# Kernel optimization log

Measured on AMD Instinct MI355X. Metric: run time of the kernel, lower is better.

Reference implementation:

```python
import jax, jax.numpy as jnp
import numpy as np


def setup_inputs() -> dict:
    key = jax.random.key(0)
    ks = jax.random.split(key, 6)
    B, C1, C2, C, H, W = 16, 512, 320, 256, 64, 64
    x1 = jax.random.normal(ks[0], (B, C1, H, W), dtype=jnp.float32)
    x2 = jax.random.normal(ks[1], (B, C2, H, W), dtype=jnp.float32)
    # 1x1 conv weights, bias=False -> plain channel matmuls
    w_img = jax.random.normal(ks[2], (C, C1), dtype=jnp.float32) * (1.0 / np.sqrt(C1))
    w_txt = jax.random.normal(ks[3], (C, C2), dtype=jnp.float32) * (1.0 / np.sqrt(C2))
    w_out = jax.random.normal(ks[4], (C1, C), dtype=jnp.float32) * (1.0 / np.sqrt(C))
    gamma = jax.random.normal(ks[5], (1,), dtype=jnp.float32)
    return {"x1": x1, "x2": x2, "w_img": w_img, "w_txt": w_txt,
            "w_out": w_out, "gamma": gamma}


def reference(x1, x2, w_img, w_txt, w_out, gamma):
    B, _, H, W = x1.shape
    # 1x1 conv projections (bias-free) == channel matmuls
    img = jnp.einsum('oc,bchw->bohw', w_img, x1)   # [B,C,H,W]
    txt = jnp.einsum('oc,bchw->bohw', w_txt, x2)   # [B,C,H,W]
    C = img.shape[1]
    q = img.reshape(B, C, H * W)                    # [B,C,N]
    kv = txt.reshape(B, C, H * W)                   # [B,C,N]
    attn = jnp.einsum('bcn,bdn->bcd', q, kv)        # QK^T over spatial dim
    attn = jax.nn.softmax(attn, axis=-1)            # [B,C,C]
    attn_info = jnp.einsum('bcd,bdn->bcn', attn, kv).reshape(B, C, H, W)
    out = gamma[0] * attn_info + img                # scale-residual
    out = jnp.einsum('oc,bchw->bohw', w_out, out)   # output 1x1 conv
    return out
```

## Files before the change

kernel.cpp:

```cpp
#include <hip/hip_runtime.h>
#include <stdint.h>

typedef _Float16 f16_t;
typedef _Float16 f16x4 __attribute__((ext_vector_type(4)));
typedef _Float16 f16x8 __attribute__((ext_vector_type(8)));
typedef float f32x4 __attribute__((ext_vector_type(4)));

__device__ __forceinline__ void async16(const void* g, void* lds) {
    typedef __attribute__((address_space(3))) void lds_void;
    typedef __attribute__((address_space(1))) void glb_void;
    lds_void* l = (lds_void*)(unsigned int)(unsigned long long)lds;
    glb_void* gp = (glb_void*)(unsigned long long)g;
    __builtin_amdgcn_global_load_lds(gp, l, 16, 0, 0);
}

__global__ void cvt3(const float* __restrict__ a, f16_t* __restrict__ oa, int na,
                     const float* __restrict__ b, f16_t* __restrict__ ob, int nb,
                     const float* __restrict__ c, f16_t* __restrict__ oc, int nc) {
    int i = blockIdx.x * 256 + threadIdx.x;
    if (i < na) oa[i] = (f16_t)a[i];
    if (i < nb) ob[i] = (f16_t)b[i];
    if (i < nc) oc[i] = (f16_t)c[i];
}

template <int BM, int BN, int TM, int TN, int WM, int WN, int MODE, int KSPLIT, int FUSET>
__global__ __launch_bounds__(256, 2)
void gemm_bt(const f16_t* __restrict__ A, const f16_t* __restrict__ B16,
             const float* __restrict__ Bf32,
             void* __restrict__ C, const f16_t* __restrict__ resid,
             const float* __restrict__ gamma, f16_t* __restrict__ Ct,
             int M, int N, int K,
             long long strideA, long long strideB, long long strideC,
             long long strideCt) {
    constexpr int BK = 32;
    static_assert(FUSET == 0 || (BN == 128), "fused path assumes BN=128");
    constexpr int ASZ = BM * BK;
    constexpr int BSZ = BN * BK;
    constexpr int STG = 2 * ASZ + 2 * BSZ;
    constexpr int LT = (MODE == 3) ? BN * (BM + 8) : 0;
    constexpr int POOL = (STG > LT) ? STG : LT;
    __shared__ __align__(16) f16_t pool[POOL];

    const int tid = threadIdx.x;
    const int wave = tid >> 6;
    const int lane = tid & 63;
    const int wm = wave / WN;
    const int wn = wave % WN;
    const int l16 = lane & 15;
    const int l4 = lane >> 4;

    const long long zb = (KSPLIT == 1) ? blockIdx.z : (blockIdx.z / KSPLIT);
    const int ks = (KSPLIT == 1) ? 0 : (blockIdx.z % KSPLIT);
    const int Ksl = K / KSPLIT;
    const f16_t* Ab = A + zb * strideA + (long long)blockIdx.y * BM * K;
    const f16_t* Bb = (FUSET == 0) ? (B16 + zb * strideB + (long long)blockIdx.x * BN * K) : nullptr;
    const float* BfB = FUSET ? (Bf32 + zb * strideB + blockIdx.x * BN) : nullptr;

    f32x4 zero = {0.f, 0.f, 0.f, 0.f};
    f32x4 acc[TM][TN];
#pragma unroll
    for (int i = 0; i < TM; ++i)
#pragma unroll
        for (int j = 0; j < TN; ++j) acc[i][j] = zero;

    auto stageA = [&](int b, int k0) {
        f16_t* As = pool + b * ASZ;
#pragma unroll
        for (int r = 0; r < (BM * 4) / 256; ++r) {
            int seg = r * 256 + tid;
            const f16_t* g = Ab + (long long)(seg >> 2) * K + k0 + (seg & 3) * 8;
            async16(g, &As[(r * 256 + wave * 64) * 8]);
        }
    };
    auto stageB16 = [&](int b, int k0) {
#pragma unroll
        for (int r = 0; r < (BN * 4) / 256; ++r) {
            int seg = r * 256 + tid;
            const f16_t* g = Bb + (long long)(seg >> 2) * K + k0 + (seg & 3) * 8;
            async16(g, &pool[2 * ASZ + b * BSZ + (r * 256 + wave * 64) * 8]);
        }
    };
    float4 br[4];
    const int fk = tid >> 3;
    const int fc = (tid & 7) * 4;
    const int fswz = ((fk >> 3) & 3) * 8;
    auto loadB = [&](int k0) {
#pragma unroll
        for (int i = 0; i < 4; ++i)
            br[i] = *(const float4*)(BfB + (long long)(k0 + fk) * N + fc + i * 32);
    };
    auto writeB = [&](int b) {
        f16_t* Bs = pool + 2 * ASZ + b * BSZ;
#pragma unroll
        for (int i = 0; i < 4; ++i) {
            int n4 = fc + i * 32;
            f16x4 h;
            h[0] = (f16_t)br[i].x; h[1] = (f16_t)br[i].y;
            h[2] = (f16_t)br[i].z; h[3] = (f16_t)br[i].w;
            *(f16x4*)&Bs[fk * BN + (n4 ^ fswz)] = h;
        }
    };

    auto compute = [&](int b) {
        const f16_t* As = pool + b * ASZ;
        f16x8 af[TM], bfr[TN];
#pragma unroll
        for (int i = 0; i < TM; ++i)
            af[i] = *(const f16x8*)&As[((wm * TM + i) * 16 + l16) * BK + l4 * 8];
        if (FUSET) {
            const f16_t* Bs = pool + 2 * ASZ + b * BSZ;
#pragma unroll
            for (int j = 0; j < TN; ++j) {
                const int nj = ((wn * TN + j) * 16 + l16) ^ (l4 * 8);
                f16x8 t;
#pragma unroll
                for (int e = 0; e < 8; ++e)
                    t[e] = Bs[(l4 * 8 + e) * BN + nj];
                bfr[j] = t;
            }
        } else {
            const f16_t* Bs = pool + 2 * ASZ + b * BSZ;
#pragma unroll
            for (int j = 0; j < TN; ++j)
                bfr[j] = *(const f16x8*)&Bs[((wn * TN + j) * 16 + l16) * BK + l4 * 8];
        }
#pragma unroll
        for (int i = 0; i < TM; ++i)
#pragma unroll
            for (int j = 0; j < TN; ++j)
                acc[i][j] = __builtin_amdgcn_mfma_f32_16x16x32_f16(af[i], bfr[j], acc[i][j], 0, 0, 0);
    };

    const int kBeg = ks * Ksl;
    const int NT = Ksl / BK;
    int cur = 0;
    if (FUSET) {
        loadB(kBeg);
        stageA(0, kBeg);
        writeB(0);
        __syncthreads();
        for (int t = 1; t < NT; ++t) {
            loadB(kBeg + t * BK);
            stageA(cur ^ 1, kBeg + t * BK);
            compute(cur);
            writeB(cur ^ 1);
            __syncthreads();
            cur ^= 1;
        }
        compute(cur);
    } else {
        stageA(0, kBeg);
        stageB16(0, kBeg);
        __syncthreads();
        for (int t = 1; t < NT; ++t) {
            stageA(cur ^ 1, kBeg + t * BK);
            stageB16(cur ^ 1, kBeg + t * BK);
            compute(cur);
            __syncthreads();
            cur ^= 1;
        }
        compute(cur);
    }

    if (MODE == 3) __syncthreads();

    const int row0 = blockIdx.y * BM + wm * TM * 16;
    const int col0 = blockIdx.x * BN + wn * TN * 16;
    float g = (MODE == 2) ? gamma[0] : 0.f;
#pragma unroll
    for (int i = 0; i < TM; ++i) {
#pragma unroll
        for (int j = 0; j < TN; ++j) {
            f16x4 tq;
#pragma unroll
            for (int r = 0; r < 4; ++r) {
                int row = row0 + i * 16 + l4 * 4 + r;
                int col = col0 + j * 16 + l16;
                float v = acc[i][j][r];
                if (MODE == 4) {
                    long long idx = (long long)blockIdx.z * strideC + (long long)row * N + col;
                    ((float*)C)[idx] = v;
                } else {
                    long long idx = zb * strideC + (long long)row * N + col;
                    if (MODE == 0) {
                        ((f16_t*)C)[idx] = (f16_t)v;
                    } else if (MODE == 1) {
                        ((float*)C)[idx] = v;
                    } else if (MODE == 2) {
                        float im = (float)resid[idx];
                        ((f16_t*)C)[idx] = (f16_t)(g * v + im);
                    } else if (MODE == 3) {
                        ((f16_t*)C)[idx] = (f16_t)v;
                        tq[r] = (f16_t)v;
                    }
                }
            }
            if (MODE == 3) {
                int rl = wm * (TM * 16) + i * 16 + l4 * 4;
                int cl = wn * (TN * 16) + j * 16 + l16;
                *(f16x4*)&pool[cl * (BM + 8) + rl] = tq;
            }
        }
    }

    if (MODE == 3) {
        __syncthreads();
        const int bx0 = blockIdx.x * BN;
        const int by0 = blockIdx.y * BM;
        const long long cb = zb * strideCt;
        constexpr int TPR = BM / 8;
        constexpr int RPI = 256 / TPR;
#pragma unroll
        for (int it = 0; it < BN / RPI; ++it) {
            int nl = it * RPI + (tid / TPR);
            int c8 = (tid % TPR) * 8;
            f16x8 v = *(const f16x8*)&pool[nl * (BM + 8) + c8];
            *(f16x8*)&Ct[cb + (long long)(bx0 + nl) * M + by0 + c8] = v;
        }
    }
}

template <int KS>
__global__ void softmax_red(const float* __restrict__ part, f16_t* __restrict__ out) {
    const int row = blockIdx.x * 4 + (threadIdx.x >> 6);
    const int lane = threadIdx.x & 63;
    const int b = row >> 8, r = row & 255;
    const float* p = part + (long long)(b * KS) * 65536 + r * 256 + lane * 4;
    float4 v = *(const float4*)p;
#pragma unroll
    for (int k = 1; k < KS; ++k) {
        float4 u = *(const float4*)(p + (long long)k * 65536);
        v.x += u.x; v.y += u.y; v.z += u.z; v.w += u.w;
    }
    float m = fmaxf(fmaxf(v.x, v.y), fmaxf(v.z, v.w));
#pragma unroll
    for (int off = 32; off > 0; off >>= 1) m = fmaxf(m, __shfl_xor(m, off, 64));
    float e0 = __expf(v.x - m), e1 = __expf(v.y - m);
    float e2 = __expf(v.z - m), e3 = __expf(v.w - m);
    float s = e0 + e1 + e2 + e3;
#pragma unroll
    for (int off = 32; off > 0; off >>= 1) s += __shfl_xor(s, off, 64);
    const float inv = 1.0f / s;
    f16x4 o;
    o[0] = (f16_t)(e0 * inv);
    o[1] = (f16_t)(e1 * inv);
    o[2] = (f16_t)(e2 * inv);
    o[3] = (f16_t)(e3 * inv);
    *(f16x4*)(out + ((long long)row) * 256 + lane * 4) = o;
}

extern "C" void kernel_launch(void* const* d_in, const int* in_sizes, int n_in,
                              void* d_out, int out_size, void* d_ws, size_t ws_size,
                              hipStream_t stream) {
    (void)in_sizes; (void)n_in; (void)out_size; (void)ws_size;

    const float* x1 = (const float*)d_in[0];
    const float* x2 = (const float*)d_in[1];
    const float* w_img = (const float*)d_in[2];
    const float* w_txt = (const float*)d_in[3];
    const float* w_out = (const float*)d_in[4];
    const float* gamma = (const float*)d_in[5];

    constexpr int B = 16, C1 = 512, C2 = 320, C = 256, N = 4096, OC = 512;
    constexpr int KS = 8;
    constexpr long long NC = (long long)N * C;
    constexpr long long CC = (long long)C * C;

    char* ws = (char*)d_ws;
    f16_t* wib   = (f16_t*)(ws + 0);
    f16_t* wtb   = (f16_t*)(ws + 262144);
    f16_t* wob   = (f16_t*)(ws + 425984);
    f16_t* img   = (f16_t*)(ws + 688128);
    f16_t* imgT  = (f16_t*)(ws + 34242560);
    f16_t* kvT   = (f16_t*)(ws + 67796992);
    f16_t* attns = (f16_t*)(ws + 101351424);
    f16_t* yT    = img;

    char* oc = (char*)d_out;
    f16_t* kv   = (f16_t*)(oc);
    float* part = (float*)(oc + 33554432);

    cvt3<<<512, 256, 0, stream>>>(w_img, wib, C * C1, w_txt, wtb, C * C2, w_out, wob, OC * C);

    gemm_bt<256, 128, 8, 4, 2, 2, 3, 1, 1><<<dim3(N / 128, 1, B), 256, 0, stream>>>(
        wib, nullptr, x1, img, nullptr, nullptr, imgT, C, N, C1,
        0LL, (long long)C1 * N, NC, NC);

    gemm_bt<256, 128, 8, 4, 2, 2, 3, 1, 1><<<dim3(N / 128, 1, B), 256, 0, stream>>>(
        wtb, nullptr, x2, kv, nullptr, nullptr, kvT, C, N, C2,
        0LL, (long long)C2 * N, NC, NC);

    gemm_bt<128, 128, 4, 4, 2, 2, 4, KS, 0><<<dim3(C / 128, C / 128, B * KS), 256, 0, stream>>>(
        img, kv, nullptr, part, nullptr, nullptr, nullptr, C, C, N,
        NC, NC, CC, 0LL);

    softmax_red<KS><<<(B * C) / 4, 256, 0, stream>>>(part, attns);

    gemm_bt<128, 128, 4, 4, 2, 2, 2, 1, 0><<<dim3(C / 128, N / 128, B), 256, 0, stream>>>(
        kvT, attns, nullptr, yT, imgT, gamma, nullptr, N, C, C,
        NC, CC, NC, 0LL);

    gemm_bt<256, 128, 8, 4, 2, 2, 1, 1, 0><<<dim3(N / 128, OC / 256, B), 256, 0, stream>>>(
        wob, yT, nullptr, (float*)d_out, nullptr, nullptr, nullptr, OC, N, C,
        0LL, NC, (long long)OC * N, 0LL);
}
```

Measured before the change: 391.9 us.

## Fuse projection GEMMs, convert weights in-kernel, raise K-split, shrink tiles

Replaces the separate weight-conversion kernel with in-GEMM fp32-to-fp16 loading of the A operand, and merges the image and text projection GEMMs into one launch with 128x128 tiles. The QK^T split-K factor goes from 8 to 16 and the output GEMM uses 128-row tiles. Occupancy hint rises to 3 blocks per CU. The aim is fewer launches and more parallel blocks. The cost is that weights are reconverted per block in registers, the A tile in LDS is written unswizzled, and the split-K partials double the reduction traffic.

```diff
diff --git a/kernel.cpp b/kernel.cpp
--- a/kernel.cpp
+++ b/kernel.cpp
@@ -14,32 +14,21 @@
     __builtin_amdgcn_global_load_lds(gp, l, 16, 0, 0);
 }
 
-__global__ void cvt3(const float* __restrict__ a, f16_t* __restrict__ oa, int na,
-                     const float* __restrict__ b, f16_t* __restrict__ ob, int nb,
-                     const float* __restrict__ c, f16_t* __restrict__ oc, int nc) {
-    int i = blockIdx.x * 256 + threadIdx.x;
-    if (i < na) oa[i] = (f16_t)a[i];
-    if (i < nb) ob[i] = (f16_t)b[i];
-    if (i < nc) oc[i] = (f16_t)c[i];
-}
-
-template <int BM, int BN, int TM, int TN, int WM, int WN, int MODE, int KSPLIT, int FUSET>
-__global__ __launch_bounds__(256, 2)
-void gemm_bt(const f16_t* __restrict__ A, const f16_t* __restrict__ B16,
-             const float* __restrict__ Bf32,
-             void* __restrict__ C, const f16_t* __restrict__ resid,
-             const float* __restrict__ gamma, f16_t* __restrict__ Ct,
-             int M, int N, int K,
-             long long strideA, long long strideB, long long strideC,
-             long long strideCt) {
+template <int BM, int BN, int TM, int TN, int WM, int WN, int MODE, int FA, int FB>
+__device__ __forceinline__ void gemm_core(
+    const void* __restrict__ Aop,
+    const void* __restrict__ Bop,
+    void* __restrict__ C,
+    const f16_t* __restrict__ resid,
+    const float* __restrict__ gamma,
+    f16_t* __restrict__ Ct,
+    int ldC, int ldCt, int ldA, int ldB,
+    int kBeg, int kEnd, int row0b, int col0b,
+    f16_t* __restrict__ pool) {
     constexpr int BK = 32;
-    static_assert(FUSET == 0 || (BN == 128), "fused path assumes BN=128");
     constexpr int ASZ = BM * BK;
     constexpr int BSZ = BN * BK;
-    constexpr int STG = 2 * ASZ + 2 * BSZ;
-    constexpr int LT = (MODE == 3) ? BN * (BM + 8) : 0;
-    constexpr int POOL = (STG > LT) ? STG : LT;
-    __shared__ __align__(16) f16_t pool[POOL];
+    static_assert(FB == 0 || BN == 128, "fused-B path assumes BN=128");
 
     const int tid = threadIdx.x;
     const int wave = tid >> 6;
@@ -49,12 +38,10 @@
     const int l16 = lane & 15;
     const int l4 = lane >> 4;
 
-    const long long zb = (KSPLIT == 1) ? blockIdx.z : (blockIdx.z / KSPLIT);
-    const int ks = (KSPLIT == 1) ? 0 : (blockIdx.z % KSPLIT);
-    const int Ksl = K / KSPLIT;
-    const f16_t* Ab = A + zb * strideA + (long long)blockIdx.y * BM * K;
-    const f16_t* Bb = (FUSET == 0) ? (B16 + zb * strideB + (long long)blockIdx.x * BN * K) : nullptr;
-    const float* BfB = FUSET ? (Bf32 + zb * strideB + blockIdx.x * BN) : nullptr;
+    const f16_t* A16 = (const f16_t*)Aop;
+    const float* A32 = (const float*)Aop;
+    const f16_t* B16 = (const f16_t*)Bop;
+    const float* B32 = (const float*)Bop;
 
     f32x4 zero = {0.f, 0.f, 0.f, 0.f};
     f32x4 acc[TM][TN];
@@ -63,52 +50,79 @@
 #pragma unroll
         for (int j = 0; j < TN; ++j) acc[i][j] = zero;
 
+    float4 ar[FA ? 4 : 1];
+    auto loadA = [&](int k0) {
+        if (FA) {
+#pragma unroll
+            for (int s = 0; s < 4; ++s) {
+                int seg = s * 256 + tid;
+                ar[s] = *(const float4*)(A32 + (long long)(seg >> 3) * ldA + k0 + (seg & 7) * 4);
+            }
+        }
+    };
+    auto writeA = [&](int b) {
+        if (FA) {
+            f16_t* As = pool + b * ASZ;
+#pragma unroll
+            for (int s = 0; s < 4; ++s) {
+                int seg = s * 256 + tid;
+                f16x4 h;
+                h[0] = (f16_t)ar[s].x; h[1] = (f16_t)ar[s].y;
+                h[2] = (f16_t)ar[s].z; h[3] = (f16_t)ar[s].w;
+                *(f16x4*)&As[(seg >> 3) * BK + (seg & 7) * 4] = h;
+            }
+        }
+    };
     auto stageA = [&](int b, int k0) {
         f16_t* As = pool + b * ASZ;
 #pragma unroll
         for (int r = 0; r < (BM * 4) / 256; ++r) {
             int seg = r * 256 + tid;
-            const f16_t* g = Ab + (long long)(seg >> 2) * K + k0 + (seg & 3) * 8;
+            const f16_t* g = A16 + (long long)(seg >> 2) * ldA + k0 + (seg & 3) * 8;
             async16(g, &As[(r * 256 + wave * 64) * 8]);
         }
     };
-    auto stageB16 = [&](int b, int k0) {
-#pragma unroll
-        for (int r = 0; r < (BN * 4) / 256; ++r) {
-            int seg = r * 256 + tid;
-            const f16_t* g = Bb + (long long)(seg >> 2) * K + k0 + (seg & 3) * 8;
-            async16(g, &pool[2 * ASZ + b * BSZ + (r * 256 + wave * 64) * 8]);
-        }
-    };
-    float4 br[4];
+    float4 br[FB ? 4 : 1];
     const int fk = tid >> 3;
     const int fc = (tid & 7) * 4;
     const int fswz = ((fk >> 3) & 3) * 8;
     auto loadB = [&](int k0) {
-#pragma unroll
-        for (int i = 0; i < 4; ++i)
-            br[i] = *(const float4*)(BfB + (long long)(k0 + fk) * N + fc + i * 32);
+        if (FB) {
+#pragma unroll
+            for (int i = 0; i < 4; ++i)
+                br[i] = *(const float4*)(B32 + (long long)(k0 + fk) * ldB + fc + i * 32);
+        }
     };
     auto writeB = [&](int b) {
-        f16_t* Bs = pool + 2 * ASZ + b * BSZ;
-#pragma unroll
-        for (int i = 0; i < 4; ++i) {
-            int n4 = fc + i * 32;
-            f16x4 h;
-            h[0] = (f16_t)br[i].x; h[1] = (f16_t)br[i].y;
-            h[2] = (f16_t)br[i].z; h[3] = (f16_t)br[i].w;
-            *(f16x4*)&Bs[fk * BN + (n4 ^ fswz)] = h;
+        if (FB) {
+            f16_t* Bs = pool + 2 * ASZ + b * BSZ;
+#pragma unroll
+            for (int i = 0; i < 4; ++i) {
+                int n4 = fc + i * 32;
+                f16x4 h;
+                h[0] = (f16_t)br[i].x; h[1] = (f16_t)br[i].y;
+                h[2] = (f16_t)br[i].z; h[3] = (f16_t)br[i].w;
+                *(f16x4*)&Bs[fk * BN + (n4 ^ fswz)] = h;
+            }
+        }
+    };
+    auto stageB = [&](int b, int k0) {
+#pragma unroll
+        for (int r = 0; r < (BN * 4) / 256; ++r) {
+            int seg = r * 256 + tid;
+            const f16_t* g = B16 + (long long)(seg >> 2) * ldB + k0 + (seg & 3) * 8;
+            async16(g, &pool[2 * ASZ + b * BSZ + (r * 256 + wave * 64) * 8]);
         }
     };
 
     auto compute = [&](int b) {
         const f16_t* As = pool + b * ASZ;
+        const f16_t* Bs = pool + 2 * ASZ + b * BSZ;
         f16x8 af[TM], bfr[TN];
 #pragma unroll
         for (int i = 0; i < TM; ++i)
             af[i] = *(const f16x8*)&As[((wm * TM + i) * 16 + l16) * BK + l4 * 8];
-        if (FUSET) {
-            const f16_t* Bs = pool + 2 * ASZ + b * BSZ;
+        if (FB) {
 #pragma unroll
             for (int j = 0; j < TN; ++j) {
                 const int nj = ((wn * TN + j) * 16 + l16) ^ (l4 * 8);
@@ -119,7 +133,6 @@
                 bfr[j] = t;
             }
         } else {
-            const f16_t* Bs = pool + 2 * ASZ + b * BSZ;
 #pragma unroll
             for (int j = 0; j < TN; ++j)
                 bfr[j] = *(const f16x8*)&Bs[((wn * TN + j) * 16 + l16) * BK + l4 * 8];
@@ -131,42 +144,30 @@
                 acc[i][j] = __builtin_amdgcn_mfma_f32_16x16x32_f16(af[i], bfr[j], acc[i][j], 0, 0, 0);
     };
 
-    const int kBeg = ks * Ksl;
-    const int NT = Ksl / BK;
+    const int NT = (kEnd - kBeg) / BK;
     int cur = 0;
-    if (FUSET) {
-        loadB(kBeg);
-        stageA(0, kBeg);
-        writeB(0);
+    if (FA) loadA(kBeg); else stageA(0, kBeg);
+    if (FB) loadB(kBeg); else stageB(0, kBeg);
+    writeA(0);
+    writeB(0);
+    __syncthreads();
+    for (int t = 1; t < NT; ++t) {
+        const int k0 = kBeg + t * BK;
+        if (FA) loadA(k0); else stageA(cur ^ 1, k0);
+        if (FB) loadB(k0); else stageB(cur ^ 1, k0);
+        compute(cur);
+        writeA(cur ^ 1);
+        writeB(cur ^ 1);
         __syncthreads();
-        for (int t = 1; t < NT; ++t) {
-            loadB(kBeg + t * BK);
-            stageA(cur ^ 1, kBeg + t * BK);
-            compute(cur);
-            writeB(cur ^ 1);
-            __syncthreads();
-            cur ^= 1;
-        }
-        compute(cur);
-    } else {
-        stageA(0, kBeg);
-        stageB16(0, kBeg);
-        __syncthreads();
-        for (int t = 1; t < NT; ++t) {
-            stageA(cur ^ 1, kBeg + t * BK);
-            stageB16(cur ^ 1, kBeg + t * BK);
-            compute(cur);
-            __syncthreads();
-            cur ^= 1;
-        }
-        compute(cur);
+        cur ^= 1;
     }
+    compute(cur);
 
     if (MODE == 3) __syncthreads();
 
-    const int row0 = blockIdx.y * BM + wm * TM * 16;
-    const int col0 = blockIdx.x * BN + wn * TN * 16;
-    float g = (MODE == 2) ? gamma[0] : 0.f;
+    const int row0 = row0b + wm * TM * 16;
+    const int col0 = col0b + wn * TN * 16;
+    const float g = (MODE == 2) ? gamma[0] : 0.f;
 #pragma unroll
     for (int i = 0; i < TM; ++i) {
 #pragma unroll
@@ -176,23 +177,18 @@
             for (int r = 0; r < 4; ++r) {
                 int row = row0 + i * 16 + l4 * 4 + r;
                 int col = col0 + j * 16 + l16;
+                long long idx = (long long)row * ldC + col;
                 float v = acc[i][j][r];
-                if (MODE == 4) {
-                    long long idx = (long long)blockIdx.z * strideC + (long long)row * N + col;
+                if (MODE == 0) {
+                    ((f16_t*)C)[idx] = (f16_t)v;
+                } else if (MODE == 1) {
                     ((float*)C)[idx] = v;
-                } else {
-                    long long idx = zb * strideC + (long long)row * N + col;
-                    if (MODE == 0) {
-                        ((f16_t*)C)[idx] = (f16_t)v;
-                    } else if (MODE == 1) {
-                        ((float*)C)[idx] = v;
-                    } else if (MODE == 2) {
-                        float im = (float)resid[idx];
-                        ((f16_t*)C)[idx] = (f16_t)(g * v + im);
-                    } else if (MODE == 3) {
-                        ((f16_t*)C)[idx] = (f16_t)v;
-                        tq[r] = (f16_t)v;
-                    }
+                } else if (MODE == 2) {
+                    float im = (float)resid[idx];
+                    ((f16_t*)C)[idx] = (f16_t)(g * v + im);
+                } else if (MODE == 3) {
+                    ((f16_t*)C)[idx] = (f16_t)v;
+                    tq[r] = (f16_t)v;
                 }
             }
             if (MODE == 3) {
@@ -205,9 +201,6 @@
 
     if (MODE == 3) {
         __syncthreads();
-        const int bx0 = blockIdx.x * BN;
-        const int by0 = blockIdx.y * BM;
-        const long long cb = zb * strideCt;
         constexpr int TPR = BM / 8;
         constexpr int RPI = 256 / TPR;
 #pragma unroll
@@ -215,9 +208,77 @@
             int nl = it * RPI + (tid / TPR);
             int c8 = (tid % TPR) * 8;
             f16x8 v = *(const f16x8*)&pool[nl * (BM + 8) + c8];
-            *(f16x8*)&Ct[cb + (long long)(bx0 + nl) * M + by0 + c8] = v;
+            *(f16x8*)&Ct[(long long)(col0b + nl) * ldCt + row0b + c8] = v;
         }
     }
+}
+
+__global__ __launch_bounds__(256, 3) void g12(
+    const float* __restrict__ x1, const float* __restrict__ x2,
+    const float* __restrict__ w_img, const float* __restrict__ w_txt,
+    f16_t* __restrict__ img, f16_t* __restrict__ imgT,
+    f16_t* __restrict__ kv, f16_t* __restrict__ kvT) {
+    __shared__ __align__(16) f16_t pool[128 * (128 + 8)];
+    const int z = blockIdx.z;
+    const bool is1 = z < 16;
+    const int b = is1 ? z : z - 16;
+    const int K = is1 ? 512 : 320;
+    const float* A = is1 ? w_img : w_txt;
+    const float* Bf = (is1 ? x1 : x2) + (long long)b * K * 4096;
+    f16_t* C = (is1 ? img : kv) + (long long)b * (256LL * 4096);
+    f16_t* Ct = (is1 ? imgT : kvT) + (long long)b * (4096LL * 256);
+    const int row0 = blockIdx.y * 128;
+    const int col0 = blockIdx.x * 128;
+    gemm_core<128, 128, 4, 4, 2, 2, 3, 1, 1>(
+        A + (long long)row0 * K, Bf + col0,
+        C, nullptr, nullptr, Ct,
+        4096, 256, K, 4096, 0, K, row0, col0, pool);
+}
+
+__global__ __launch_bounds__(256, 3) void g3(
+    const f16_t* __restrict__ img, const f16_t* __restrict__ kv,
+    float* __restrict__ part) {
+    __shared__ __align__(16) f16_t pool[4 * 128 * 32];
+    const int z = blockIdx.z;
+    const int b = z >> 4, ks = z & 15;
+    const int row0 = blockIdx.y * 128;
+    const int col0 = blockIdx.x * 128;
+    const long long NC = 256LL * 4096;
+    gemm_core<128, 128, 4, 4, 2, 2, 1, 0, 0>(
+        img + b * NC + (long long)row0 * 4096,
+        kv + b * NC + (long long)col0 * 4096,
+        part + (long long)z * 65536, nullptr, nullptr, nullptr,
+        256, 0, 4096, 4096, ks * 256, ks * 256 + 256, row0, col0, pool);
+}
+
+__global__ __launch_bounds__(256, 3) void g4(
+    const f16_t* __restrict__ kvT, const f16_t* __restrict__ attns,
+    const f16_t* __restrict__ imgT, const float* __restrict__ gamma,
+    f16_t* __restrict__ yT) {
+    __shared__ __align__(16) f16_t pool[4 * 128 * 32];
+    const int b = blockIdx.z;
+    const int row0 = blockIdx.y * 128;
+    const int col0 = blockIdx.x * 128;
+    const long long NC = 4096LL * 256;
+    gemm_core<128, 128, 4, 4, 2, 2, 2, 0, 0>(
+        kvT + b * NC + (long long)row0 * 256,
+        attns + b * 65536LL + (long long)col0 * 256,
+        yT + b * NC, imgT + b * NC, gamma, nullptr,
+        256, 0, 256, 256, 0, 256, row0, col0, pool);
+}
+
+__global__ __launch_bounds__(256, 3) void g5(
+    const float* __restrict__ w_out, const f16_t* __restrict__ yT,
+    float* __restrict__ out) {
+    __shared__ __align__(16) f16_t pool[4 * 128 * 32];
+    const int b = blockIdx.z;
+    const int row0 = blockIdx.y * 128;
+    const int col0 = blockIdx.x * 128;
+    gemm_core<128, 128, 4, 4, 2, 2, 1, 1, 0>(
+        w_out + (long long)row0 * 256,
+        yT + b * (4096LL * 256) + (long long)col0 * 256,
+        out + b * (512LL * 4096), nullptr, nullptr, nullptr,
+        4096, 0, 256, 256, 0, 256, row0, col0, pool);
 }
 
 template <int KS>
@@ -261,46 +322,24 @@
     const float* w_out = (const float*)d_in[4];
     const float* gamma = (const float*)d_in[5];
 
-    constexpr int B = 16, C1 = 512, C2 = 320, C = 256, N = 4096, OC = 512;
-    constexpr int KS = 8;
-    constexpr long long NC = (long long)N * C;
-    constexpr long long CC = (long long)C * C;
-
     char* ws = (char*)d_ws;
-    f16_t* wib   = (f16_t*)(ws + 0);
-    f16_t* wtb   = (f16_t*)(ws + 262144);
-    f16_t* wob   = (f16_t*)(ws + 425984);
-    f16_t* img   = (f16_t*)(ws + 688128);
-    f16_t* imgT  = (f16_t*)(ws + 34242560);
-    f16_t* kvT   = (f16_t*)(ws + 67796992);
-    f16_t* attns = (f16_t*)(ws + 101351424);
+    f16_t* img   = (f16_t*)(ws + 0);
+    f16_t* imgT  = (f16_t*)(ws + 33554432);
+    f16_t* kvT   = (f16_t*)(ws + 67108864);
+    f16_t* attns = (f16_t*)(ws + 100663296);
     f16_t* yT    = img;
 
     char* oc = (char*)d_out;
-    f16_t* kv   = (f16_t*)(oc);
+    f16_t* kv   = (f16_t*)oc;
     float* part = (float*)(oc + 33554432);
 
-    cvt3<<<512, 256, 0, stream>>>(w_img, wib, C * C1, w_txt, wtb, C * C2, w_out, wob, OC * C);
-
-    gemm_bt<256, 128, 8, 4, 2, 2, 3, 1, 1><<<dim3(N / 128, 1, B), 256, 0, stream>>>(
-        wib, nullptr, x1, img, nullptr, nullptr, imgT, C, N, C1,
-        0LL, (long long)C1 * N, NC, NC);
-
-    gemm_bt<256, 128, 8, 4, 2, 2, 3, 1, 1><<<dim3(N / 128, 1, B), 256, 0, stream>>>(
-        wtb, nullptr, x2, kv, nullptr, nullptr, kvT, C, N, C2,
-        0LL, (long long)C2 * N, NC, NC);
-
-    gemm_bt<128, 128, 4, 4, 2, 2, 4, KS, 0><<<dim3(C / 128, C / 128, B * KS), 256, 0, stream>>>(
-        img, kv, nullptr, part, nullptr, nullptr, nullptr, C, C, N,
-        NC, NC, CC, 0LL);
-
-    softmax_red<KS><<<(B * C) / 4, 256, 0, stream>>>(part, attns);
-
-    gemm_bt<128, 128, 4, 4, 2, 2, 2, 1, 0><<<dim3(C / 128, N / 128, B), 256, 0, stream>>>(
-        kvT, attns, nullptr, yT, imgT, gamma, nullptr, N, C, C,
-        NC, CC, NC, 0LL);
-
-    gemm_bt<256, 128, 8, 4, 2, 2, 1, 1, 0><<<dim3(N / 128, OC / 256, B), 256, 0, stream>>>(
-        wob, yT, nullptr, (float*)d_out, nullptr, nullptr, nullptr, OC, N, C,
-        0LL, NC, (long long)OC * N, 0LL);
-}
+    g12<<<dim3(32, 2, 32), 256, 0, stream>>>(x1, x2, w_img, w_txt, img, imgT, kv, kvT);
+
+    g3<<<dim3(2, 2, 256), 256, 0, stream>>>(img, kv, part);
+
+    softmax_red<16><<<1024, 256, 0, stream>>>(part, attns);
+
+    g4<<<dim3(2, 32, 16), 256, 0, stream>>>(kvT, attns, imgT, gamma, yT);
+
+    g5<<<dim3(32, 4, 16), 256, 0, stream>>>(w_out, yT, (float*)d_out);
+}
```

Result: slower. 435.6 us (+11.1%).
